# Performance work log

Hardware: AMD Instinct MI355X
Metric: run time of the kernel (lower is better)

## Reference

```python
import jax, jax.numpy as jnp
import numpy as np

MAX_DISP = 128.0  # self.max_disparity


def _warp_horizontal(img, disp, sign):
    """Horizontal-only bilinear warp, equivalent to F.grid_sample with
    align_corners=True, padding_mode='border' and an exact integer y-grid
    (so vertical interpolation is identity).
    img: [B,C,H,W], disp: [B,H,W]; sign=-1 -> xx - disp (left_to_right),
    sign=+1 -> xx + disp (right_to_left)."""
    B, C, H, W = img.shape
    xx = jnp.arange(W, dtype=img.dtype)
    x = xx[None, None, :] + sign * disp              # [B,H,W] sample x-coords
    x = jnp.clip(x, 0.0, W - 1)                      # border padding
    x0 = jnp.floor(x)
    w1 = x - x0                                      # right-neighbor weight
    i0 = x0.astype(jnp.int32)
    i1 = jnp.minimum(i0 + 1, W - 1)
    i0b = jnp.broadcast_to(i0[:, None, :, :], (B, C, H, W))
    i1b = jnp.broadcast_to(i1[:, None, :, :], (B, C, H, W))
    v0 = jnp.take_along_axis(img, i0b, axis=3)
    v1 = jnp.take_along_axis(img, i1b, axis=3)
    w1c = w1[:, None, :, :]
    return v0 * (1.0 - w1c) + v1 * w1c


def setup_inputs() -> dict:
    key = jax.random.key(0)
    k1, k2, k3 = jax.random.split(key, 3)
    B, C, H, W = 8, 3, 1024, 1920
    img_l = jax.random.uniform(k1, (B, C, H, W), dtype=jnp.float32)
    img_r = jax.random.uniform(k2, (B, C, H, W), dtype=jnp.float32)
    depth_map = jax.random.uniform(k3, (B, 1, H, W), dtype=jnp.float32)
    return {"img_l": img_l, "img_r": img_r, "depth_map": depth_map}


def reference(img_l, img_r, depth_map):
    # depth_to_disparity: disparity = clamp(depth * max_disparity, 0, max_disparity)
    disp = jnp.clip(depth_map * MAX_DISP, 0.0, MAX_DISP)[:, 0]  # [B,H,W]
    warped_r = _warp_horizontal(img_r, disp, -1.0)  # left_to_right: xx - disp
    warped_l = _warp_horizontal(img_l, disp, +1.0)  # right_to_left: xx + disp
    denoised_l = (img_l + warped_r) * 0.5
    denoised_r = (img_r + warped_l) * 0.5
    return denoised_l, denoised_r
```

## Files before the change

kernel.cpp:

```cpp
#include <hip/hip_runtime.h>


constexpr int B = 8, C = 3, H = 1024, W = 1920;
constexpr int HW  = H * W;
constexpr int CHW = C * HW;
constexpr int W4  = W / 4;
constexpr long OUT_HALF = (long)B * CHW;
constexpr float MAX_DISP = 128.0f;

__global__ __launch_bounds__(256) void stereo_denoise(
    const float* __restrict__ img_l, const float* __restrict__ img_r,
    const float* __restrict__ depth, float* __restrict__ out)
{
    int tid = blockIdx.x * blockDim.x + threadIdx.x;
    if (tid >= B * H * W4) return;

    int w4 = tid % W4;
    int bh = tid / W4;
    int b  = bh / H;
    int w  = w4 * 4;
    long row = (long)bh * W;

    const float4 d4 = *reinterpret_cast<const float4*>(depth + row + w);
    float dispv[4] = {d4.x, d4.y, d4.z, d4.w};

    int   i0m[4], i1m[4], i0p[4], i1p[4];
    float wm[4], wp[4];
#pragma unroll
    for (int j = 0; j < 4; ++j) {
        float d  = fminf(fmaxf(dispv[j] * MAX_DISP, 0.0f), MAX_DISP);
        float xw = (float)(w + j);
        float xm = fminf(fmaxf(xw - d, 0.0f), (float)(W - 1));
        float xp = fminf(fmaxf(xw + d, 0.0f), (float)(W - 1));
        float fm  = floorf(xm);
        float fpp = floorf(xp);
        i0m[j] = (int)fm;  i1m[j] = min(i0m[j] + 1, W - 1);  wm[j] = xm - fm;
        i0p[j] = (int)fpp; i1p[j] = min(i0p[j] + 1, W - 1);  wp[j] = xp - fpp;
    }

    long base = row + (long)(2 * b) * HW;

#pragma unroll
    for (int c = 0; c < C; ++c) {
        const float* pl = img_l + base + (long)c * HW;
        const float* pr = img_r + base + (long)c * HW;

        float4 vl = *reinterpret_cast<const float4*>(pl + w);
        float4 vr = *reinterpret_cast<const float4*>(pr + w);
        const float* vlp = &vl.x;
        const float* vrp = &vr.x;

        float4 ol, orr;
        float* olp = &ol.x;
        float* orp = &orr.x;
#pragma unroll
        for (int j = 0; j < 4; ++j) {
            float r0 = pr[i0m[j]], r1 = pr[i1m[j]];
            float warped_r = r0 * (1.0f - wm[j]) + r1 * wm[j];
            float l0 = pl[i0p[j]], l1 = pl[i1p[j]];
            float warped_l = l0 * (1.0f - wp[j]) + l1 * wp[j];
            olp[j] = (vlp[j] + warped_r) * 0.5f;
            orp[j] = (vrp[j] + warped_l) * 0.5f;
        }
        long oidx = base + (long)c * HW + w;
        *reinterpret_cast<float4*>(out + oidx)            = ol;
        *reinterpret_cast<float4*>(out + OUT_HALF + oidx) = orr;
    }
}

extern "C" void kernel_launch(void* const* d_in, const int* in_sizes, int n_in,
                              void* d_out, int out_size, void* d_ws, size_t ws_size,
                              hipStream_t stream) {
    const float* img_l = (const float*)d_in[0];
    const float* img_r = (const float*)d_in[1];
    const float* depth = (const float*)d_in[2];
    float* out = (float*)d_out;

    const int total = B * H * W4;
    const int block = 256;
    const int grid  = (total + block - 1) / block;
    stereo_denoise<<<grid, block, 0, stream>>>(img_l, img_r, depth, out);
}
```

Before: 681.1 us.

## Stage full image rows in LDS and gather warp samples from shared memory

Each block now handles one (batch,row) pair and cooperatively loads all six channel rows of both images into LDS with float4 loads. The bilinear gathers then read from LDS instead of scattered global reads, and a zeroed pad element replaces the i1 clamp, since its weight is zero when x sits on the last column. This aims to remove redundant and uncoalesced global gather traffic. In exchange it adds about 46KB of LDS per block and a block-wide sync, which can limit occupancy, and 32 of the 512 threads sit idle during the compute phase.

```diff
diff --git a/kernel.cpp b/kernel.cpp
--- a/kernel.cpp
+++ b/kernel.cpp
@@ -4,46 +4,58 @@
 constexpr int B = 8, C = 3, H = 1024, W = 1920;
 constexpr int HW  = H * W;
 constexpr int CHW = C * HW;
-constexpr int W4  = W / 4;
 constexpr long OUT_HALF = (long)B * CHW;
 constexpr float MAX_DISP = 128.0f;
+constexpr int W4 = W / 4;
+constexpr int LSTRIDE = W + 4;
 
-__global__ __launch_bounds__(256) void stereo_denoise(
+__global__ __launch_bounds__(512) void stereo_denoise(
     const float* __restrict__ img_l, const float* __restrict__ img_r,
     const float* __restrict__ depth, float* __restrict__ out)
 {
-    int tid = blockIdx.x * blockDim.x + threadIdx.x;
-    if (tid >= B * H * W4) return;
+    __shared__ float lds[6 * LSTRIDE];
 
-    int w4 = tid % W4;
-    int bh = tid / W4;
-    int b  = bh / H;
-    int w  = w4 * 4;
-    long row = (long)bh * W;
+    const int tid = threadIdx.x;
+    const int bh  = blockIdx.x;
+    const int b   = bh >> 10;
+    const long rowD = (long)bh * W;
+    const long rowI = rowD + (long)(2 * b) * HW;
 
-    const float4 d4 = *reinterpret_cast<const float4*>(depth + row + w);
-    float dispv[4] = {d4.x, d4.y, d4.z, d4.w};
+    for (int i = tid; i < 6 * W4; i += 512) {
+        int p  = i / W4;
+        int c4 = i - p * W4;
+        const float* src = (p < 3 ? img_l : img_r)
+                         + rowI + (long)(p < 3 ? p : p - 3) * HW + c4 * 4;
+        *reinterpret_cast<float4*>(&lds[p * LSTRIDE + c4 * 4]) =
+            *reinterpret_cast<const float4*>(src);
+    }
+    if (tid < 6) lds[tid * LSTRIDE + W] = 0.0f;
+    __syncthreads();
 
-    int   i0m[4], i1m[4], i0p[4], i1p[4];
+    if (tid >= W4) return;
+    const int w = tid * 4;
+
+    const float4 d4 = *reinterpret_cast<const float4*>(depth + rowD + w);
+    const float dv[4] = {d4.x, d4.y, d4.z, d4.w};
+
+    int   i0m[4], i0p[4];
     float wm[4], wp[4];
 #pragma unroll
     for (int j = 0; j < 4; ++j) {
-        float d  = fminf(fmaxf(dispv[j] * MAX_DISP, 0.0f), MAX_DISP);
+        float d  = fminf(fmaxf(dv[j] * MAX_DISP, 0.0f), MAX_DISP);
         float xw = (float)(w + j);
         float xm = fminf(fmaxf(xw - d, 0.0f), (float)(W - 1));
         float xp = fminf(fmaxf(xw + d, 0.0f), (float)(W - 1));
         float fm  = floorf(xm);
-        float fpp = floorf(xp);
-        i0m[j] = (int)fm;  i1m[j] = min(i0m[j] + 1, W - 1);  wm[j] = xm - fm;
-        i0p[j] = (int)fpp; i1p[j] = min(i0p[j] + 1, W - 1);  wp[j] = xp - fpp;
+        float fp2 = floorf(xp);
+        i0m[j] = (int)fm;  wm[j] = xm - fm;
+        i0p[j] = (int)fp2; wp[j] = xp - fp2;
     }
-
-    long base = row + (long)(2 * b) * HW;
 
 #pragma unroll
     for (int c = 0; c < C; ++c) {
-        const float* pl = img_l + base + (long)c * HW;
-        const float* pr = img_r + base + (long)c * HW;
+        const float* pl = &lds[c * LSTRIDE];
+        const float* pr = &lds[(3 + c) * LSTRIDE];
 
         float4 vl = *reinterpret_cast<const float4*>(pl + w);
         float4 vr = *reinterpret_cast<const float4*>(pr + w);
@@ -55,14 +67,14 @@
         float* orp = &orr.x;
 #pragma unroll
         for (int j = 0; j < 4; ++j) {
-            float r0 = pr[i0m[j]], r1 = pr[i1m[j]];
+            float r0 = pr[i0m[j]], r1 = pr[i0m[j] + 1];
+            float l0 = pl[i0p[j]], l1 = pl[i0p[j] + 1];
             float warped_r = r0 * (1.0f - wm[j]) + r1 * wm[j];
-            float l0 = pl[i0p[j]], l1 = pl[i1p[j]];
             float warped_l = l0 * (1.0f - wp[j]) + l1 * wp[j];
             olp[j] = (vlp[j] + warped_r) * 0.5f;
             orp[j] = (vrp[j] + warped_l) * 0.5f;
         }
-        long oidx = base + (long)c * HW + w;
+        long oidx = rowI + (long)c * HW + w;
         *reinterpret_cast<float4*>(out + oidx)            = ol;
         *reinterpret_cast<float4*>(out + OUT_HALF + oidx) = orr;
     }
@@ -76,8 +88,7 @@
     const float* depth = (const float*)d_in[2];
     float* out = (float*)d_out;
 
-    const int total = B * H * W4;
-    const int block = 256;
-    const int grid  = (total + block - 1) / block;
+    const int grid  = B * H;
+    const int block = 512;
     stereo_denoise<<<grid, block, 0, stream>>>(img_l, img_r, depth, out);
 }
```

Measured after the change: 634.1 us. 6.9% less time.
